# Performance work log

Measured on AMD Instinct MI355X. Metric: run time of the kernel, lower is better.

The kernel has to match this reference:

```python
import jax, jax.numpy as jnp
import numpy as np
from jax import lax

IMG = 224.0
IOU_THRESH = 0.5

def box_cxcywh_to_xyxy(b):
    cx, cy, w, h = b[..., 0], b[..., 1], b[..., 2], b[..., 3]
    return jnp.stack([cx - 0.5 * w, cy - 0.5 * h, cx + 0.5 * w, cy + 0.5 * h], axis=-1)

def box_iou(a, b):
    area_a = (a[:, 2] - a[:, 0]) * (a[:, 3] - a[:, 1])
    area_b = (b[:, 2] - b[:, 0]) * (b[:, 3] - b[:, 1])
    lt = jnp.maximum(a[:, None, :2], b[None, :, :2])
    rb = jnp.minimum(a[:, None, 2:], b[None, :, 2:])
    wh = jnp.clip(rb - lt, 0.0)
    inter = wh[..., 0] * wh[..., 1]
    return inter / (area_a[:, None] + area_b[None, :] - inter)

def gumbel_softmax(key, logits, axis, tau=1.0):
    # straight-through hard gumbel-softmax (matches torch hard=True)
    g = jax.random.gumbel(key, logits.shape, logits.dtype)
    y = jax.nn.softmax((logits + g) / tau, axis=axis)
    y_hard = jax.nn.one_hot(jnp.argmax(y, axis=axis), y.shape[axis], axis=axis, dtype=y.dtype)
    return y + lax.stop_gradient(y_hard - y)

def nms_indices(boxes, scores, thresh):
    # iterative greedy NMS, returns kept indices in descending-score order (as torchvision)
    n = boxes.shape[0]
    order = jnp.argsort(-scores)
    b = boxes[order]
    areas = (b[:, 2] - b[:, 0]) * (b[:, 3] - b[:, 1])
    pos = jnp.arange(n)
    def body(i, suppressed):
        bi = b[i]
        lt = jnp.maximum(bi[:2], b[:, :2])
        rb = jnp.minimum(bi[2:], b[:, 2:])
        wh = jnp.clip(rb - lt, 0.0)
        inter = wh[:, 0] * wh[:, 1]
        iou = inter / (areas[i] + areas - inter)
        sup = (iou > thresh) & (pos > i) & jnp.logical_not(suppressed[i])
        return suppressed | sup
    suppressed = lax.fori_loop(0, n, body, jnp.zeros((n,), bool))
    keep = np.asarray(jnp.logical_not(suppressed))
    return jnp.asarray(np.asarray(order)[keep])

def _keys():
    return jax.random.split(jax.random.key(42), 3)

def _boxes_and_scores(classencodings, pred_logits, pred_boxes, tgt_ids, batch_idx, tgt_bbox, k0):
    C = classencodings.shape[0]
    B, Q, D = pred_logits.shape
    similarity = jnp.einsum('bqd,cd->bqc', pred_logits, classencodings)
    out_scores = jnp.max(similarity, axis=-1)
    clt = gumbel_softmax(k0, similarity, axis=-1)                      # [B,Q,C] hard
    offx = jnp.arange(C, dtype=pred_logits.dtype) * IMG
    offy = jnp.arange(B, dtype=pred_logits.dtype) * IMG
    ox = jnp.sum(clt * offx, axis=-1)                                  # [B,Q]
    oy = jnp.broadcast_to(offy[:, None], (B, Q))
    out_off = jnp.tile(jnp.stack([ox, oy], axis=-1), (1, 1, 2))        # [B,Q,4]
    out_bbox = (box_cxcywh_to_xyxy(pred_boxes) + out_off).reshape(-1, 4)
    f = pred_logits.dtype
    gt_off = jnp.tile(jnp.stack([IMG * tgt_ids.astype(f), IMG * batch_idx.astype(f)], axis=-1), (1, 2))
    tb = box_cxcywh_to_xyxy(tgt_bbox) + gt_off                         # [N,4]
    return similarity, out_scores.reshape(-1), out_bbox, tb

def ce_diag(logits):
    # CrossEntropyLoss(mean) with targets arange(n)
    return -jnp.mean(jnp.diagonal(jax.nn.log_softmax(logits, axis=1)))

def _forward(classencodings, pred_logits, pred_boxes, pred_masks, tgt_masks, tgt_embs, tgt_bbox, tgt_ids, batch_idx, nms_idx):
    k0, k1, k2 = _keys()
    B, Q, D = pred_logits.shape
    N = tgt_embs.shape[0]
    W, H = tgt_masks.shape[-2:]
    similarity, out_scores, out_bbox, tb = _boxes_and_scores(classencodings, pred_logits, pred_boxes, tgt_ids, batch_idx, tgt_bbox, k0)
    kept = out_bbox[nms_idx]                                           # [K,4]
    K = kept.shape[0]
    iou = box_iou(kept, tb)
    iou = jnp.where(jnp.isnan(iou), 0.0, iou)
    gt_log = jax.nn.softmax(iou, axis=1)
    gt_one_hot = gumbel_softmax(k1, gt_log, axis=1)                    # [K,N]
    gt_sel = gt_one_hot.T @ kept                                       # [N,4]
    gt_ious = jnp.diagonal(box_iou(gt_sel, tb))
    out_embs = gt_one_hot.T @ pred_logits.reshape(-1, D)[nms_idx]      # [N,D]
    class_loss = ce_diag(tgt_embs @ out_embs.T) + ce_diag(out_embs @ tgt_embs.T)
    scores = jnp.einsum('bqd,nd->bqn', pred_logits, tgt_embs).reshape(B * Q, N)
    ind = gumbel_softmax(k2, scores, axis=0).T                         # [N,B*Q]
    om = (ind @ pred_masks.reshape(B * Q, -1)).reshape(N, W, H)
    overall_mask_loss = jnp.mean((om - tgt_masks) ** 2)
    ocm = jnp.einsum('qwh,bcq->bcwh', om, similarity) / om.shape[1]    # [B,Q,W,H] (N==C==Q)
    ocm = jax.nn.softmax(ocm, axis=1)
    batch_lookup = jax.nn.one_hot(batch_idx, B, dtype=pred_logits.dtype).T  # [B,N]
    gt_sim = tgt_embs @ classencodings.T                               # [N,C]
    tsim = batch_lookup[:, :, None] * gt_sim[None, :, :]               # [B,N,C]
    gt_cm = jnp.einsum('bnc,nwh->bcwh', tsim, tgt_masks)               # [B,C,W,H]
    inp = ocm.reshape(B, -1)
    tgt = gt_cm.reshape(B, -1)
    dice = jnp.mean(jnp.sum(inp * tgt) / (jnp.sum(inp, -1) + jnp.sum(tgt, -1) + 1e-6))
    l1 = jnp.abs(gt_sel - tb).sum()
    return jnp.stack([class_loss, dice, overall_mask_loss / K, (1.0 - gt_ious).sum() / K, l1 / K])

def setup_inputs():
    key = jax.random.key(0)
    ks = jax.random.split(key, 10)
    B, Q, C, N, D, W, H = 8, 300, 300, 300, 256, 96, 96
    return {
        'classencodings': jax.random.normal(ks[0], (C, D), jnp.float32),
        'pred_logits': jax.random.normal(ks[1], (B, Q, D), jnp.float32),
        'pred_boxes': jax.random.uniform(ks[2], (B, Q, 4), jnp.float32),
        'pred_masks': jax.random.normal(ks[3], (B * Q, W, H), jnp.float32),
        'tgt_masks': jax.random.uniform(ks[4], (N, W, H), jnp.float32),
        'tgt_embs': jax.random.normal(ks[5], (N, D), jnp.float32),
        'tgt_bbox': jax.random.uniform(ks[6], (N, 4), jnp.float32),
        'im_masks': jnp.ones((B, 224, 224), jnp.float32),
        'tgt_ids': jax.random.randint(ks[7], (N,), 0, C, jnp.int32),
        'batch_idx': jnp.sort(jax.random.randint(ks[8], (N,), 0, B, jnp.int32)),
    }

def reference(classencodings, pred_logits, pred_boxes, pred_masks, tgt_masks, tgt_embs, tgt_bbox, im_masks, tgt_ids, batch_idx):
    k0, _, _ = _keys()
    _, scores, out_bbox, _ = _boxes_and_scores(classencodings, pred_logits, pred_boxes, tgt_ids, batch_idx, tgt_bbox, k0)
    nms_idx = nms_indices(out_bbox, scores, IOU_THRESH)
    return _forward(classencodings, pred_logits, pred_boxes, pred_masks, tgt_masks, tgt_embs, tgt_bbox, tgt_ids, batch_idx, nms_idx)
```

## Files before the change

kernel.cpp:

```cpp
#include <hip/hip_runtime.h>
#include <stdint.h>

#define DEVFN __device__ __forceinline__

typedef unsigned short u16;
typedef short bf16x8 __attribute__((ext_vector_type(8)));
typedef float f32x4 __attribute__((ext_vector_type(4)));

constexpr int BB = 8, QQ = 300, CC = 300, NN = 300, DD = 256;
constexpr int WHX = 9216, BQ = 2400, SIMW = 600;
constexpr int QP = 320;
constexpr int CP = 304;
constexpr int KP = 96;
constexpr int NP = 416;
constexpr int CELLCAP = 300;

constexpr size_t F_SIMS   = 0;
constexpr size_t F_GTSIM  = F_SIMS   + (size_t)BQ*SIMW;
constexpr size_t F_MM     = F_GTSIM  + (size_t)NN*CC;
constexpr size_t F_SCORE  = F_MM     + (size_t)NN*NN;
constexpr size_t F_BBOX   = F_SCORE  + BQ;
constexpr size_t F_TB     = F_BBOX   + (size_t)BQ*4;
constexpr size_t F_SB     = F_TB     + (size_t)NN*4;
constexpr size_t F_SAREA  = F_SB     + (size_t)BQ*4;
constexpr size_t F_KB     = F_SAREA  + BQ;
constexpr size_t F_ROWSUM = F_KB     + (size_t)BQ*4;
constexpr size_t F_OE     = F_ROWSUM + NN;
constexpr size_t F_GSEL   = F_OE     + (size_t)NN*DD;
constexpr size_t F_MSUM   = F_GSEL   + (size_t)NN*4;
constexpr size_t F_STGT   = F_MSUM   + NN;
constexpr size_t F_SC     = F_STGT   + 8;
constexpr size_t F_CNT    = F_SC     + 16;
constexpr size_t F_ACCEND = F_CNT    + BQ;
constexpr size_t F_ORDER  = F_ACCEND;
constexpr size_t F_NMSIDX = F_ORDER  + BQ;
constexpr size_t F_SEL2   = F_NMSIDX + BQ;
constexpr size_t F_BSTART = F_SEL2   + NN;
constexpr size_t F_KINT   = F_BSTART + 16;
constexpr size_t F_CLS    = F_KINT   + 4;
constexpr size_t F_KEEPF  = F_CLS    + BQ;
constexpr size_t F_LIST   = F_KEEPF  + BQ;
constexpr size_t F_S2T    = F_LIST   + (size_t)BQ*CELLCAP;
constexpr size_t F_SIMTB  = ((F_S2T + (size_t)NN*BQ + 7) & ~(size_t)7);
constexpr size_t F_OMT    = F_SIMTB + (size_t)BB*CP*QP/2;
constexpr size_t F_TMT    = F_OMT   + (size_t)WHX*QP/2;
constexpr size_t F_GTP    = F_TMT   + (size_t)WHX*NP/2;
constexpr size_t F_TOTAL  = F_GTP   + (size_t)BB*CP*KP/2;

DEVFN uint32_t rotl32(uint32_t v, int r){ return (v << r) | (v >> (32 - r)); }

DEVFN void tf2x32(uint32_t k0, uint32_t k1, uint32_t x0, uint32_t x1,
                  uint32_t& o0, uint32_t& o1){
  uint32_t ks2 = k0 ^ k1 ^ 0x1BD11BDAu;
  x0 += k0; x1 += k1;
#define TFR(r) x0 += x1; x1 = rotl32(x1, r); x1 ^= x0;
  TFR(13) TFR(15) TFR(26) TFR(6)   x0 += k1;  x1 += ks2 + 1u;
  TFR(17) TFR(29) TFR(16) TFR(24)  x0 += ks2; x1 += k0  + 2u;
  TFR(13) TFR(15) TFR(26) TFR(6)   x0 += k0;  x1 += k1  + 3u;
  TFR(17) TFR(29) TFR(16) TFR(24)  x0 += k1;  x1 += ks2 + 4u;
  TFR(13) TFR(15) TFR(26) TFR(6)   x0 += ks2; x1 += k0  + 5u;
#undef TFR
  o0 = x0; o1 = x1;
}

DEVFN void subkey(int i, uint32_t& k0, uint32_t& k1){
  tf2x32(0u, 42u, 0u, (uint32_t)i, k0, k1);
}

DEVFN float gumbel32(uint32_t k0, uint32_t k1, uint32_t idx){
  uint32_t h, l; tf2x32(k0, k1, 0u, idx, h, l);
  uint32_t bits = h ^ l;
  float f = __uint_as_float((bits >> 9) | 0x3F800000u) - 1.0f;
  const float tiny = 1.17549435e-38f;
  float u = fmaxf(tiny, f + tiny);
  return -logf(-logf(u));
}

DEVFN float iou_xyxy(float ax1,float ay1,float ax2,float ay2,
                     float bx1,float by1,float bx2,float by2){
  float aa = (ax2-ax1)*(ay2-ay1);
  float ab = (bx2-bx1)*(by2-by1);
  float lx = fmaxf(ax1,bx1), ly = fmaxf(ay1,by1);
  float rx = fminf(ax2,bx2), ry = fminf(ay2,by2);
  float iw = fmaxf(rx-lx,0.f), ih = fmaxf(ry-ly,0.f);
  float in_ = iw*ih;
  return in_/(aa+ab-in_);
}

DEVFN u16 f2bf(float x){
  uint32_t u = __float_as_uint(x);
  uint32_t r = u + 0x7FFFu + ((u >> 16) & 1u);
  return (u16)(r >> 16);
}

DEVFN void gload_lds16(const u16* g, u16* l){
  __builtin_amdgcn_global_load_lds(
      (const __attribute__((address_space(1))) unsigned int*)g,
      (__attribute__((address_space(3))) unsigned int*)l,
      16, 0, 0);
}

__global__ __launch_bounds__(256) void k_gemm_t(
    const float* __restrict__ pl, const float* __restrict__ ce,
    const float* __restrict__ te, float* __restrict__ sims,
    float* __restrict__ gtsim, float* __restrict__ s2t){
  __shared__ float As[16][64];
  __shared__ float Bs[16][64];
  const int row0 = blockIdx.x * 64, col0 = blockIdx.y * 64;
  const int tid = threadIdx.x;
  const int lrow = tid >> 2, lk0 = (tid & 3) * 4;
  const int tr = tid >> 4, tc = tid & 15;

  float acc[4][4];
  #pragma unroll
  for (int i = 0; i < 4; i++)
    #pragma unroll
    for (int j = 0; j < 4; j++) acc[i][j] = 0.f;

  const float4 z4 = {0.f,0.f,0.f,0.f};
  const int grow = row0 + lrow;
  const int gcol = col0 + lrow;
  const float* arow = nullptr;
  if (grow < 2400) arow = pl + (size_t)grow * DD;
  else if (grow < 2700) arow = te + (size_t)(grow - 2400) * DD;
  const float* brow = nullptr;
  if (gcol < 300) brow = ce + (size_t)gcol * DD;
  else if (gcol < 600) brow = te + (size_t)(gcol - 300) * DD;

  float4 av = arow ? *(const float4*)(arow + lk0) : z4;
  float4 bv = brow ? *(const float4*)(brow + lk0) : z4;

  for (int step = 0; step < 16; step++){
    __syncthreads();
    #pragma unroll
    for (int j = 0; j < 4; j++){
      As[lk0 + j][lrow] = ((const float*)&av)[j];
      Bs[lk0 + j][lrow] = ((const float*)&bv)[j];
    }
    __syncthreads();
    if (step + 1 < 16){
      const int k0 = (step + 1) * 16;
      av = arow ? *(const float4*)(arow + k0 + lk0) : z4;
      bv = brow ? *(const float4*)(brow + k0 + lk0) : z4;
    }
    #pragma unroll
    for (int kk = 0; kk < 16; kk++){
      float4 a4 = *(const float4*)&As[kk][tr*4];
      float4 b4 = *(const float4*)&Bs[kk][tc*4];
      float a[4] = {a4.x,a4.y,a4.z,a4.w};
      float b[4] = {b4.x,b4.y,b4.z,b4.w};
      #pragma unroll
      for (int i = 0; i < 4; i++)
        #pragma unroll
        for (int j = 0; j < 4; j++)
          acc[i][j] = fmaf(a[i], b[j], acc[i][j]);
    }
  }

  #pragma unroll
  for (int i = 0; i < 4; i++){
    const int r = row0 + tr*4 + i;
    const int c0 = col0 + tc*4;
    if (r < 2400){
      if (c0 < 600){
        float4 o0 = {acc[i][0],acc[i][1],acc[i][2],acc[i][3]};
        *(float4*)(sims + (size_t)r*SIMW + c0) = o0;
        if (c0 >= 300){
          #pragma unroll
          for (int j = 0; j < 4; j++)
            s2t[(size_t)(c0 + j - 300)*BQ + r] = acc[i][j];
        }
      }
    } else if (r < 2700){
      const int n = r - 2400;
      #pragma unroll
      for (int j = 0; j < 4; j++){
        int c = c0 + j;
        if (c < 300) gtsim[(size_t)n*CC + c] = acc[i][j];
      }
    }
  }
}

__global__ __launch_bounds__(256) void k_post(
    const float* __restrict__ sims, const float* __restrict__ pb,
    const float* __restrict__ tbb, const int* __restrict__ tids,
    const int* __restrict__ bidx, const float* __restrict__ gtsim,
    float* __restrict__ score, float* __restrict__ bbox,
    float* __restrict__ tb, float* __restrict__ rowsum,
    int* __restrict__ clsout){
  int bq = blockIdx.x, tid = threadIdx.x;
  __shared__ float sv[256];
  __shared__ int   si[256];
  const int i2 = tid + 256;
  float v1 = (tid < CC) ? sims[(size_t)bq*SIMW + tid] : -INFINITY;
  float v2 = (i2  < CC) ? sims[(size_t)bq*SIMW + i2]  : -INFINITY;
  sv[tid] = fmaxf(v1, v2); __syncthreads();
  for (int s = 128; s > 0; s >>= 1){ if (tid < s) sv[tid] = fmaxf(sv[tid], sv[tid+s]); __syncthreads(); }
  if (tid == 0) score[bq] = sv[0];
  __syncthreads();
  uint32_t gk0, gk1; subkey(0, gk0, gk1);
  float y1 = (tid < CC) ? v1 + gumbel32(gk0, gk1, (uint32_t)(bq*CC + tid)) : -INFINITY;
  float y2 = (i2  < CC) ? v2 + gumbel32(gk0, gk1, (uint32_t)(bq*CC + i2))  : -INFINITY;
  float ym; int yi;
  if (y2 > y1){ ym = y2; yi = i2; } else { ym = y1; yi = tid; }
  sv[tid] = ym; si[tid] = yi; __syncthreads();
  for (int s = 128; s > 0; s >>= 1){
    if (tid < s){
      float ov = sv[tid+s]; int oi = si[tid+s];
      if (ov > sv[tid] || (ov == sv[tid] && oi < si[tid])){ sv[tid] = ov; si[tid] = oi; }
    }
    __syncthreads();
  }
  if (tid == 0){
    int cls = si[0];
    clsout[bq] = cls;
    float ox = 224.0f * (float)cls;
    float oy = 224.0f * (float)(bq / QQ);
    float cx = pb[bq*4+0], cy = pb[bq*4+1], ww = pb[bq*4+2], hh = pb[bq*4+3];
    bbox[bq*4+0] = cx - 0.5f*ww + ox;
    bbox[bq*4+1] = cy - 0.5f*hh + oy;
    bbox[bq*4+2] = cx + 0.5f*ww + ox;
    bbox[bq*4+3] = cy + 0.5f*hh + oy;
  }
  if (bq < NN){
    __syncthreads();
    float r1 = (tid < CC) ? gtsim[(size_t)bq*CC + tid] : 0.f;
    float r2 = (i2  < CC) ? gtsim[(size_t)bq*CC + i2]  : 0.f;
    sv[tid] = r1 + r2; __syncthreads();
    for (int s = 128; s > 0; s >>= 1){ if (tid < s) sv[tid] += sv[tid+s]; __syncthreads(); }
    if (tid == 0) rowsum[bq] = sv[0];
    if (tid == 1){
      float gx = 224.0f * (float)tids[bq], gy = 224.0f * (float)bidx[bq];
      float cx = tbb[bq*4+0], cy = tbb[bq*4+1], ww = tbb[bq*4+2], hh = tbb[bq*4+3];
      tb[bq*4+0] = cx - 0.5f*ww + gx;
      tb[bq*4+1] = cy - 0.5f*hh + gy;
      tb[bq*4+2] = cx + 0.5f*ww + gx;
      tb[bq*4+3] = cy + 0.5f*hh + gy;
    }
  }
}

__global__ __launch_bounds__(256) void k_rankgather(
    const float* __restrict__ score, const float* __restrict__ bbox,
    const int* __restrict__ cls, const int* __restrict__ bidx,
    int* __restrict__ order, float* __restrict__ sb,
    int* __restrict__ bstart, int* __restrict__ cnt,
    int* __restrict__ list){
  const int t = blockIdx.x;
  const int tid = threadIdx.x;
  const float st = score[t];
  int c = 0;
  for (int j = tid; j < BQ; j += 256){
    float sj = score[j];
    c += (sj > st) || (sj == st && j < t);
  }
  __shared__ int red[256];
  red[tid] = c; __syncthreads();
  for (int s = 128; s > 0; s >>= 1){
    if (tid < s) red[tid] += red[tid+s];
    __syncthreads();
  }
  if (tid == 0){
    int r = red[0];
    order[r] = t;
    float x1 = bbox[t*4+0], y1 = bbox[t*4+1], x2 = bbox[t*4+2], y2 = bbox[t*4+3];
    sb[r*4+0] = x1; sb[r*4+1] = y1; sb[r*4+2] = x2; sb[r*4+3] = y2;
    int key = (t / QQ) * CC + cls[t];
    int slot = atomicAdd(&cnt[key], 1);
    list[(size_t)key*CELLCAP + slot] = r;
  }
  if (t == 0 && tid >= 32 && tid < 41){
    int b = tid - 32, cb = 0;
    for (int n = 0; n < NN; n++) cb += (bidx[n] < b);
    bstart[b] = cb;
  }
}

__global__ __launch_bounds__(256) void k_cellnms(
    const float* __restrict__ sb, const int* __restrict__ cnt,
    const int* __restrict__ list, int* __restrict__ keepf){
  int key = blockIdx.x*256 + threadIdx.x;
  if (key >= BB*CC) return;
  int m = cnt[key];
  if (m <= 0) return;
  const int* lst = list + (size_t)key*CELLCAP;
  unsigned long long keptmask = 0ull;
  int prevp = -1;
  for (int a = 0; a < m; a++){
    int pa = 0x7fffffff;
    for (int j = 0; j < m; j++){
      int pj = lst[j];
      if (pj > prevp && pj < pa) pa = pj;
    }
    prevp = pa;
    float4 A = ((const float4*)sb)[pa];
    float areaA = (A.z-A.x)*(A.w-A.y);
    bool kept = true;
    int pbprev = -1;
    for (int b2 = 0; b2 < a; b2++){
      int pb = 0x7fffffff;
      for (int j = 0; j < m; j++){
        int pj = lst[j];
        if (pj > pbprev && pj < pb) pb = pj;
      }
      pbprev = pb;
      bool keptb = (m <= 64) ? (((keptmask >> b2) & 1ull) != 0ull) : (keepf[pb] != 0);
      if (!keptb) continue;
      float4 B = ((const float4*)sb)[pb];
      float areaB = (B.z-B.x)*(B.w-B.y);
      float lx = fmaxf(A.x,B.x), ly = fmaxf(A.y,B.y);
      float rx = fminf(A.z,B.z), ry = fminf(A.w,B.w);
      float iw = fmaxf(rx-lx,0.f), ih = fmaxf(ry-ly,0.f);
      float inter = iw*ih;
      if (inter/(areaA + areaB - inter) > 0.5f){ kept = false; break; }
    }
    if (m <= 64 && kept) keptmask |= (1ull << a);
    keepf[pa] = kept ? 1 : 0;
  }
}

__global__ __launch_bounds__(256) void k_compact(
    const int* __restrict__ keepflag, const int* __restrict__ order,
    const float* __restrict__ sb, int* __restrict__ nmsidx,
    float* __restrict__ kb, int* __restrict__ kint){
  __shared__ int csum[256];
  int tid = threadIdx.x;
  int p0 = tid*10;
  int keepf[10];
  int cnt = 0;
  #pragma unroll
  for (int d = 0; d < 10; d++){
    int p = p0 + d;
    int k = 0;
    if (p < BQ) k = keepflag[p];
    keepf[d] = k; cnt += k;
  }
  csum[tid] = cnt; __syncthreads();
  for (int s = 1; s < 256; s <<= 1){
    int add = (tid >= s) ? csum[tid - s] : 0;
    __syncthreads();
    csum[tid] += add;
    __syncthreads();
  }
  int pos = csum[tid] - cnt;
  #pragma unroll
  for (int d = 0; d < 10; d++){
    if (keepf[d]){
      int p = p0 + d;
      nmsidx[pos] = order[p];
      ((float4*)kb)[pos] = ((const float4*)sb)[p];
      pos++;
    }
  }
  if (tid == 255) kint[0] = csum[255];
}

__global__ __launch_bounds__(512) void k_gtsel(
    const float* __restrict__ kb, const float* __restrict__ tb,
    const int* __restrict__ nmsidx, const float* __restrict__ pl,
    const int* __restrict__ kint, float* __restrict__ gsel,
    float* __restrict__ oe){
  int k = blockIdx.x;
  if (k >= kint[0]) return;
  int tid = threadIdx.x;
  __shared__ float sv[512];
  __shared__ int   si[512];
  float4 a = ((const float4*)kb)[k];
  float iou = -INFINITY;
  if (tid < NN){
    float4 t = ((const float4*)tb)[tid];
    iou = iou_xyxy(a.x,a.y,a.z,a.w, t.x,t.y,t.z,t.w);
    if (iou != iou) iou = 0.f;
  }
  sv[tid] = iou; __syncthreads();
  for (int s = 256; s > 0; s >>= 1){ if (tid < s) sv[tid] = fmaxf(sv[tid], sv[tid+s]); __syncthreads(); }
  float m = sv[0]; __syncthreads();
  float e = (tid < NN) ? expf(iou - m) : 0.f;
  sv[tid] = e; __syncthreads();
  for (int s = 256; s > 0; s >>= 1){ if (tid < s) sv[tid] += sv[tid+s]; __syncthreads(); }
  float S = sv[0]; __syncthreads();
  uint32_t gk0, gk1; subkey(1, gk0, gk1);
  float y = (tid < NN) ? (e / S + gumbel32(gk0, gk1, (uint32_t)(k*NN + tid))) : -INFINITY;
  sv[tid] = y; si[tid] = tid; __syncthreads();
  for (int s = 256; s > 0; s >>= 1){
    if (tid < s){
      float ov = sv[tid+s]; int oi = si[tid+s];
      if (ov > sv[tid] || (ov == sv[tid] && oi < si[tid])){ sv[tid] = ov; si[tid] = oi; }
    }
    __syncthreads();
  }
  int sel = si[0];
  if (tid < 4) atomicAdd(&gsel[sel*4 + tid], ((const float*)&a)[tid]);
  if (tid < DD) atomicAdd(&oe[(size_t)sel*DD + tid], pl[(size_t)nmsidx[k]*DD + tid]);
}

__global__ __launch_bounds__(256) void k_m_t(
    const float* __restrict__ te, const float* __restrict__ oe,
    float* __restrict__ M){
  __shared__ float As[16][32];
  __shared__ float Bs[16][32];
  const int row0 = blockIdx.x * 32, col0 = blockIdx.y * 32;
  const int tid = threadIdx.x;
  const int lr = tid >> 3, lk0 = (tid & 7) * 2;
  const int tr = tid >> 4, tc = tid & 15;
  float acc[2][2] = {{0.f,0.f},{0.f,0.f}};
  const float* arow = (row0 + lr < NN) ? te + (size_t)(row0 + lr)*DD : nullptr;
  const float* brow = (col0 + lr < NN) ? oe + (size_t)(col0 + lr)*DD : nullptr;
  for (int step = 0; step < 16; step++){
    const int k0 = step*16;
    float2 a2 = arow ? *(const float2*)(arow + k0 + lk0) : float2{0.f,0.f};
    float2 b2 = brow ? *(const float2*)(brow + k0 + lk0) : float2{0.f,0.f};
    __syncthreads();
    As[lk0][lr] = a2.x; As[lk0+1][lr] = a2.y;
    Bs[lk0][lr] = b2.x; Bs[lk0+1][lr] = b2.y;
    __syncthreads();
    #pragma unroll
    for (int kk = 0; kk < 16; kk++){
      float a0 = As[kk][tr*2], a1 = As[kk][tr*2+1];
      float b0 = Bs[kk][tc*2], b1 = Bs[kk][tc*2+1];
      acc[0][0] = fmaf(a0,b0,acc[0][0]);
      acc[0][1] = fmaf(a0,b1,acc[0][1]);
      acc[1][0] = fmaf(a1,b0,acc[1][0]);
      acc[1][1] = fmaf(a1,b1,acc[1][1]);
    }
  }
  #pragma unroll
  for (int i = 0; i < 2; i++){
    int r = row0 + tr*2 + i;
    if (r >= NN) continue;
    #pragma unroll
    for (int j = 0; j < 2; j++){
      int c = col0 + tc*2 + j;
      if (c < NN) M[(size_t)r*NN + c] = acc[i][j];
    }
  }
}

__global__ __launch_bounds__(64) void k_ce(
    const float* __restrict__ M, float* __restrict__ sc){
  int i = blockIdx.x, lane = threadIdx.x;
  float m = -INFINITY;
  for (int j = lane; j < NN; j += 64) m = fmaxf(m, M[(size_t)i*NN + j]);
  for (int o = 32; o > 0; o >>= 1) m = fmaxf(m, __shfl_xor(m, o));
  float s = 0.f;
  for (int j = lane; j < NN; j += 64) s += expf(M[(size_t)i*NN + j] - m);
  for (int o = 32; o > 0; o >>= 1) s += __shfl_xor(s, o);
  float lr = m + logf(s);
  float m2 = -INFINITY;
  for (int j = lane; j < NN; j += 64) m2 = fmaxf(m2, M[(size_t)j*NN + i]);
  for (int o = 32; o > 0; o >>= 1) m2 = fmaxf(m2, __shfl_xor(m2, o));
  float s2 = 0.f;
  for (int j = lane; j < NN; j += 64) s2 += expf(M[(size_t)j*NN + i] - m2);
  for (int o = 32; o > 0; o >>= 1) s2 += __shfl_xor(s2, o);
  float lc = m2 + logf(s2);
  if (lane == 0){
    float d = M[(size_t)i*NN + i];
    atomicAdd(&sc[0], lr - d);
    atomicAdd(&sc[1], lc - d);
  }
}

__global__ __launch_bounds__(256) void k_sel2(
    const float* __restrict__ s2t, int* __restrict__ sel2){
  int n = blockIdx.x, tid = threadIdx.x;
  uint32_t gk0, gk1; subkey(2, gk0, gk1);
  float best = -INFINITY; int bi = 0x7fffffff;
  for (int r = tid; r < BQ; r += 256){
    float v = s2t[(size_t)n*BQ + r] + gumbel32(gk0, gk1, (uint32_t)(r*NN + n));
    if (v > best){ best = v; bi = r; }
  }
  __shared__ float sv[256];
  __shared__ int   si[256];
  sv[tid] = best; si[tid] = bi; __syncthreads();
  for (int s = 128; s > 0; s >>= 1){
    if (tid < s){
      float ov = sv[tid+s]; int oi = si[tid+s];
      if (ov > sv[tid] || (ov == sv[tid] && oi < si[tid])){ sv[tid] = ov; si[tid] = oi; }
    }
    __syncthreads();
  }
  if (tid == 0) sel2[n] = si[0];
}

constexpr int PB_SIMT = 400;
constexpr int PB_OMT  = 1440;
constexpr int PB_TMT  = 1872;
constexpr int PB_GTP  = 114;
constexpr int PB_OM   = 2700;
__global__ __launch_bounds__(256) void k_pack(
    const float* __restrict__ sims, const float* __restrict__ pm,
    const float* __restrict__ tm, const float* __restrict__ gtsim,
    const int* __restrict__ sel2, const int* __restrict__ bstart,
    u16* __restrict__ simTb, u16* __restrict__ omT,
    u16* __restrict__ tmT, u16* __restrict__ gtp,
    float* __restrict__ msum, float* __restrict__ sc){
  __shared__ float ld[32][65];
  const int blk = blockIdx.x;
  const int tid = threadIdx.x;

  if (blk < PB_SIMT){
    int bx = blk % 10, by = (blk / 10) % 5, b = blk / 50;
    int q0 = bx*32, c0 = by*64;
    for (int i = tid; i < 32*64; i += 256){
      int qi = i >> 6, ci = i & 63;
      int q = q0 + qi, c = c0 + ci;
      ld[qi][ci] = (q < QQ && c < CC) ? sims[((size_t)b*QQ + q)*SIMW + c] : 0.f;
    }
    __syncthreads();
    int cloc = tid >> 2, j0 = (tid & 3)*8;
    int c = c0 + cloc;
    if (c < CP){
      u16 tmp[8];
      #pragma unroll
      for (int j = 0; j < 8; j++) tmp[j] = f2bf(ld[j0+j][cloc]);
      *(uint4*)(simTb + ((size_t)b*CP + c)*QP + q0 + j0) = *(const uint4*)tmp;
    }
  } else if (blk < PB_SIMT + PB_OMT){
    int r = blk - PB_SIMT;
    int q0 = (r % 10)*32, wh0 = (r / 10)*64;
    for (int i = tid; i < 32*64; i += 256){
      int qi = i >> 6, wi = i & 63;
      int q = q0 + qi;
      ld[qi][wi] = (q < QQ) ? pm[(size_t)sel2[q]*WHX + wh0 + wi] * (1.0f/96.0f) : 0.f;
    }
    __syncthreads();
    int wloc = tid >> 2, j0 = (tid & 3)*8;
    u16 tmp[8];
    #pragma unroll
    for (int j = 0; j < 8; j++) tmp[j] = f2bf(ld[j0+j][wloc]);
    *(uint4*)(omT + (size_t)(wh0+wloc)*QP + q0 + j0) = *(const uint4*)tmp;
  } else if (blk < PB_SIMT + PB_OMT + PB_TMT){
    int r = blk - PB_SIMT - PB_OMT;
    int n0 = (r % 13)*32, wh0 = (r / 13)*64;
    for (int i = tid; i < 32*64; i += 256){
      int ni = i >> 6, wi = i & 63;
      int n = n0 + ni;
      ld[ni][wi] = (n < NN) ? tm[(size_t)n*WHX + wh0 + wi] : 0.f;
    }
    __syncthreads();
    int wloc = tid >> 2, j0 = (tid & 3)*8;
    u16 tmp[8];
    #pragma unroll
    for (int j = 0; j < 8; j++) tmp[j] = f2bf(ld[j0+j][wloc]);
    *(uint4*)(tmT + (size_t)(wh0+wloc)*NP + n0 + j0) = *(const uint4*)tmp;
  } else if (blk < PB_SIMT + PB_OMT + PB_TMT + PB_GTP){
    int g = (blk - PB_SIMT - PB_OMT - PB_TMT)*256 + tid;
    int b = g / (CP*(KP/8));
    int rem = g - b*(CP*(KP/8));
    int c = rem / (KP/8);
    int kg = rem % (KP/8);
    int n0 = bstart[b], n1 = bstart[b+1];
    int kst = n0 & ~7;
    u16 tmp[8];
    #pragma unroll
    for (int j = 0; j < 8; j++){
      int n = kst + kg*8 + j;
      float v = (n >= n0 && n < n1 && c < CC) ? gtsim[(size_t)n*CC + c] : 0.f;
      tmp[j] = f2bf(v);
    }
    *(uint4*)(gtp + ((size_t)b*CP + c)*KP + kg*8) = *(const uint4*)tmp;
  } else {
    int nb = blk - (PB_SIMT + PB_OMT + PB_TMT + PB_GTP);
    int n = nb / 9, ch = nb % 9;
    int c0 = ch*1024 + tid*4;
    const float4 o4 = *(const float4*)(pm + (size_t)sel2[n]*WHX + c0);
    const float4 t4 = *(const float4*)(tm + (size_t)n*WHX + c0);
    float dx = o4.x-t4.x, dy = o4.y-t4.y, dz = o4.z-t4.z, dw = o4.w-t4.w;
    float d2 = dx*dx + dy*dy + dz*dz + dw*dw;
    float ts = t4.x + t4.y + t4.z + t4.w;
    float* r1 = &ld[0][0];
    float* r2 = r1 + 256;
    r1[tid] = d2; r2[tid] = ts; __syncthreads();
    for (int s = 128; s > 0; s >>= 1){
      if (tid < s){ r1[tid] += r1[tid+s]; r2[tid] += r2[tid+s]; }
      __syncthreads();
    }
    if (tid == 0){ atomicAdd(&sc[2], r1[0]); atomicAdd(&msum[n], r2[0]); }
  }
}

constexpr int ALDS = 32;
__global__ __launch_bounds__(256) void k_zsoft(
    const u16* __restrict__ simTb, const u16* __restrict__ omT,
    const u16* __restrict__ gtp, const u16* __restrict__ tmT,
    const int* __restrict__ bstart, float* __restrict__ sc){
  const int bid = blockIdx.x;
  const int xcd = bid & 7;
  const int r9  = bid >> 3;
  const int tile = xcd * 18 + (r9 % 18);
  const int b    = r9 / 18;
  const int tid = threadIdx.x;
  const int w = tid >> 6, l = tid & 63;
  const int lrow = l & 15, lgrp = l >> 4;
  const int col = tile*64 + w*16 + lrow;

  __shared__ u16 As[2][CP*ALDS];
  __shared__ float red[256];

  const u16* Ab = simTb + (size_t)b*CP*QP;
  int srcoff[5];
  #pragma unroll
  for (int i = 0; i < 5; i++){
    int p = (w*5 + i)*64 + l;
    int row = p >> 2, cs = p & 3;
    int g = cs ^ ((row >> 1) & 3);
    srcoff[i] = row*QP + g*8;
  }
  const int nIss = (w == 3) ? 4 : 5;
  const int roff = (lgrp ^ ((lrow >> 1) & 3)) << 3;
  const u16* pB = omT + (size_t)col*QP + lgrp*8;

  #pragma unroll
  for (int i = 0; i < 5; i++){
    if (i < nIss) gload_lds16(Ab + srcoff[i], &As[0][(w*5+i)*512]);
  }
  bf16x8 bcur = *(const bf16x8*)(pB);

  f32x4 acc[19];
  #pragma unroll
  for (int t = 0; t < 19; t++) acc[t] = (f32x4){0.f,0.f,0.f,0.f};
  __syncthreads();

  for (int ks = 0; ks < 10; ks++){
    const int cur = ks & 1;
    bf16x8 bnext;
    if (ks + 1 < 10){
      const int ko = (ks + 1) * 32;
      #pragma unroll
      for (int i = 0; i < 5; i++){
        if (i < nIss) gload_lds16(Ab + srcoff[i] + ko, &As[cur ^ 1][(w*5+i)*512]);
      }
      bnext = *(const bf16x8*)(pB + ko);
    }
    __builtin_amdgcn_s_setprio(1);
    #pragma unroll
    for (int t = 0; t < 19; t++){
      bf16x8 af = *(const bf16x8*)&As[cur][t*16*ALDS + lrow*ALDS + roff];
      acc[t] = __builtin_amdgcn_mfma_f32_16x16x32_bf16(af, bcur, acc[t], 0, 0, 0);
    }
    __builtin_amdgcn_s_setprio(0);
    bcur = bnext;
    __syncthreads();
  }

  float lmax = -INFINITY;
  #pragma unroll
  for (int t = 0; t < 19; t++){
    if (t == 18 && lgrp == 3) continue;
    lmax = fmaxf(lmax, fmaxf(fmaxf(acc[t][0], acc[t][1]), fmaxf(acc[t][2], acc[t][3])));
  }
  lmax = fmaxf(lmax, __shfl_xor(lmax, 16));
  lmax = fmaxf(lmax, __shfl_xor(lmax, 32));
  float ls = 0.f;
  #pragma unroll
  for (int t = 0; t < 19; t++){
    if (t == 18 && lgrp == 3){
      acc[t] = (f32x4){0.f,0.f,0.f,0.f};
      continue;
    }
    float p0 = __expf(acc[t][0] - lmax);
    float p1 = __expf(acc[t][1] - lmax);
    float p2 = __expf(acc[t][2] - lmax);
    float p3 = __expf(acc[t][3] - lmax);
    acc[t][0] = p0; acc[t][1] = p1; acc[t][2] = p2; acc[t][3] = p3;
    ls += p0 + p1 + p2 + p3;
  }
  float S = ls;
  S += __shfl_xor(S, 16);
  S += __shfl_xor(S, 32);
  float inv = 1.f / S;

  const int n0 = bstart[b];
  const int kst = n0 & ~7;
  const u16* tB = tmT + (size_t)col*NP + kst + lgrp*8;
  bf16x8 b2a = *(const bf16x8*)(tB);
  bf16x8 b2b = *(const bf16x8*)(tB + 32);
  bf16x8 b2c = *(const bf16x8*)(tB + 64);
  const u16* A2 = gtp + (size_t)b*CP*KP + (size_t)lrow*KP + lgrp*8;
  float dl = 0.f;
  #pragma unroll
  for (int t = 0; t < 19; t++){
    const u16* ar = A2 + (size_t)t*16*KP;
    f32x4 rr = (f32x4){0.f,0.f,0.f,0.f};
    rr = __builtin_amdgcn_mfma_f32_16x16x32_bf16(*(const bf16x8*)(ar),      b2a, rr, 0, 0, 0);
    rr = __builtin_amdgcn_mfma_f32_16x16x32_bf16(*(const bf16x8*)(ar + 32), b2b, rr, 0, 0, 0);
    rr = __builtin_amdgcn_mfma_f32_16x16x32_bf16(*(const bf16x8*)(ar + 64), b2c, rr, 0, 0, 0);
    dl += acc[t][0]*rr[0] + acc[t][1]*rr[1] + acc[t][2]*rr[2] + acc[t][3]*rr[3];
  }
  dl *= inv;

  red[tid] = dl; __syncthreads();
  for (int s = 128; s > 0; s >>= 1){
    if (tid < s) red[tid] += red[tid+s];
    __syncthreads();
  }
  if (tid == 0) atomicAdd(&sc[5], red[0]);
}

__global__ __launch_bounds__(512) void k_final3(
    const float* __restrict__ gsel, const float* __restrict__ tb,
    const int* __restrict__ bidx, const float* __restrict__ rowsum,
    const float* __restrict__ msum, const float* __restrict__ sc,
    const int* __restrict__ kint, float* __restrict__ out){
  int tid = threadIdx.x;
  __shared__ float s1[512], s2[512];
  __shared__ float stgt[8];
  if (tid < 8) stgt[tid] = 0.f;
  __syncthreads();
  float a1 = 0.f, a2 = 0.f;
  if (tid < NN){
    float4 g = ((const float4*)gsel)[tid];
    float4 t = ((const float4*)tb)[tid];
    float iou = iou_xyxy(g.x,g.y,g.z,g.w, t.x,t.y,t.z,t.w);
    a1 = 1.f - iou;
    a2 = fabsf(g.x-t.x) + fabsf(g.y-t.y) + fabsf(g.z-t.z) + fabsf(g.w-t.w);
    atomicAdd(&stgt[bidx[tid]], rowsum[tid] * msum[tid]);
  }
  s1[tid] = a1; s2[tid] = a2; __syncthreads();
  for (int s = 256; s > 0; s >>= 1){
    if (tid < s){ s1[tid] += s1[tid+s]; s2[tid] += s2[tid+s]; }
    __syncthreads();
  }
  if (tid == 0){
    float K = (float)kint[0];
    float cls = sc[0]/300.f + sc[1]/300.f;
    float stot = sc[5];
    float dice = 0.f;
    for (int b = 0; b < 8; b++) dice += stot / (9216.0f + stgt[b] + 1e-6f);
    dice *= (1.0f/8.0f);
    out[0] = cls;
    out[1] = dice;
    out[2] = (sc[2] / 2764800.0f) / K;
    out[3] = s1[0] / K;
    out[4] = s2[0] / K;
  }
}

extern "C" void kernel_launch(void* const* d_in, const int* in_sizes, int n_in,
                              void* d_out, int out_size, void* d_ws, size_t ws_size,
                              hipStream_t stream) {
  const float* ce  = (const float*)d_in[0];
  const float* pl  = (const float*)d_in[1];
  const float* pb  = (const float*)d_in[2];
  const float* pm  = (const float*)d_in[3];
  const float* tm  = (const float*)d_in[4];
  const float* te  = (const float*)d_in[5];
  const float* tbb = (const float*)d_in[6];
  const int*  tids = (const int*)d_in[8];
  const int*  bidx = (const int*)d_in[9];
  float* out = (float*)d_out;
  float* w = (float*)d_ws;

  if (ws_size < F_TOTAL * sizeof(float)) return;

  float* SIMS   = w + F_SIMS;
  float* GTSIM  = w + F_GTSIM;
  float* MM     = w + F_MM;
  float* SCORE  = w + F_SCORE;
  float* BBOX   = w + F_BBOX;
  float* TBOX   = w + F_TB;
  float* SB     = w + F_SB;
  float* KB     = w + F_KB;
  float* ROWSUM = w + F_ROWSUM;
  float* OE     = w + F_OE;
  float* GSEL   = w + F_GSEL;
  float* MSUM   = w + F_MSUM;
  float* SC     = w + F_SC;
  float* S2T    = w + F_S2T;
  int*   CNT    = (int*)(w + F_CNT);
  int*   ORDER  = (int*)(w + F_ORDER);
  int*   NMSIDX = (int*)(w + F_NMSIDX);
  int*   SEL2   = (int*)(w + F_SEL2);
  int*   BSTART = (int*)(w + F_BSTART);
  int*   KINT   = (int*)(w + F_KINT);
  int*   CLS    = (int*)(w + F_CLS);
  int*   KEEPF  = (int*)(w + F_KEEPF);
  int*   LIST   = (int*)(w + F_LIST);
  u16* SIMTB = (u16*)(w + F_SIMTB);
  u16* OMT   = (u16*)(w + F_OMT);
  u16* TMT   = (u16*)(w + F_TMT);
  u16* GTP   = (u16*)(w + F_GTP);

  hipMemsetAsync(w + F_OE, 0, (F_ACCEND - F_OE) * sizeof(float), stream);

  k_gemm_t<<<dim3(43, 10), 256, 0, stream>>>(pl, ce, te, SIMS, GTSIM, S2T);
  k_post<<<BQ, 256, 0, stream>>>(SIMS, pb, tbb, tids, bidx, GTSIM, SCORE, BBOX, TBOX, ROWSUM, CLS);
  k_rankgather<<<BQ, 256, 0, stream>>>(SCORE, BBOX, CLS, bidx, ORDER, SB, BSTART, CNT, LIST);
  k_sel2<<<NN, 256, 0, stream>>>(S2T, SEL2);
  k_pack<<<PB_SIMT + PB_OMT + PB_TMT + PB_GTP + PB_OM, 256, 0, stream>>>(
      SIMS, pm, tm, GTSIM, SEL2, BSTART, SIMTB, OMT, TMT, GTP, MSUM, SC);
  k_cellnms<<<(BB*CC + 255)/256, 256, 0, stream>>>(SB, CNT, LIST, KEEPF);
  k_compact<<<1, 256, 0, stream>>>(KEEPF, ORDER, SB, NMSIDX, KB, KINT);
  k_gtsel<<<BQ, 512, 0, stream>>>(KB, TBOX, NMSIDX, pl, KINT, GSEL, OE);
  k_m_t<<<dim3(10, 10), 256, 0, stream>>>(te, OE, MM);
  k_ce<<<NN, 64, 0, stream>>>(MM, SC);
  k_zsoft<<<dim3((WHX/64) * BB), 256, 0, stream>>>(SIMTB, OMT, GTP, TMT, BSTART, SC);
  k_final3<<<1, 512, 0, stream>>>(GSEL, TBOX, bidx, ROWSUM, MSUM, SC, KINT, out);
}
```

Measured before the change: 248.5 us.

## Load zsoft GEMM A-operand directly from global instead of LDS double buffer

Removes the LDS double-buffered staging of the A operand (with its XOR swizzle, async global-to-LDS copies, barriers and priority hints) in the zsoft kernel. Each wave now reads its A fragments straight from global memory per k-step. This cuts LDS traffic, barriers and LDS occupancy pressure. The cost is redundant global/L2 reads across the four waves, which previously shared the tile, and no prefetch overlap.

```diff
diff --git a/kernel.cpp b/kernel.cpp
--- a/kernel.cpp
+++ b/kernel.cpp
@@ -93,13 +93,6 @@
   return (u16)(r >> 16);
 }
 
-DEVFN void gload_lds16(const u16* g, u16* l){
-  __builtin_amdgcn_global_load_lds(
-      (const __attribute__((address_space(1))) unsigned int*)g,
-      (__attribute__((address_space(3))) unsigned int*)l,
-      16, 0, 0);
-}
-
 __global__ __launch_bounds__(256) void k_gemm_t(
     const float* __restrict__ pl, const float* __restrict__ ce,
     const float* __restrict__ te, float* __restrict__ sims,
@@ -580,7 +573,6 @@
   }
 }
 
-constexpr int ALDS = 32;
 __global__ __launch_bounds__(256) void k_zsoft(
     const u16* __restrict__ simTb, const u16* __restrict__ omT,
     const u16* __restrict__ gtp, const u16* __restrict__ tmT,
@@ -595,53 +587,23 @@
   const int lrow = l & 15, lgrp = l >> 4;
   const int col = tile*64 + w*16 + lrow;
 
-  __shared__ u16 As[2][CP*ALDS];
   __shared__ float red[256];
 
-  const u16* Ab = simTb + (size_t)b*CP*QP;
-  int srcoff[5];
-  #pragma unroll
-  for (int i = 0; i < 5; i++){
-    int p = (w*5 + i)*64 + l;
-    int row = p >> 2, cs = p & 3;
-    int g = cs ^ ((row >> 1) & 3);
-    srcoff[i] = row*QP + g*8;
-  }
-  const int nIss = (w == 3) ? 4 : 5;
-  const int roff = (lgrp ^ ((lrow >> 1) & 3)) << 3;
+  const u16* Ab = simTb + (size_t)b*CP*QP + (size_t)lrow*QP + lgrp*8;
   const u16* pB = omT + (size_t)col*QP + lgrp*8;
 
-  #pragma unroll
-  for (int i = 0; i < 5; i++){
-    if (i < nIss) gload_lds16(Ab + srcoff[i], &As[0][(w*5+i)*512]);
-  }
-  bf16x8 bcur = *(const bf16x8*)(pB);
-
   f32x4 acc[19];
   #pragma unroll
   for (int t = 0; t < 19; t++) acc[t] = (f32x4){0.f,0.f,0.f,0.f};
-  __syncthreads();
 
   for (int ks = 0; ks < 10; ks++){
-    const int cur = ks & 1;
-    bf16x8 bnext;
-    if (ks + 1 < 10){
-      const int ko = (ks + 1) * 32;
-      #pragma unroll
-      for (int i = 0; i < 5; i++){
-        if (i < nIss) gload_lds16(Ab + srcoff[i] + ko, &As[cur ^ 1][(w*5+i)*512]);
-      }
-      bnext = *(const bf16x8*)(pB + ko);
-    }
-    __builtin_amdgcn_s_setprio(1);
+    const int ko = ks * 32;
+    bf16x8 bcur = *(const bf16x8*)(pB + ko);
     #pragma unroll
     for (int t = 0; t < 19; t++){
-      bf16x8 af = *(const bf16x8*)&As[cur][t*16*ALDS + lrow*ALDS + roff];
+      bf16x8 af = *(const bf16x8*)(Ab + (size_t)t*16*QP + ko);
       acc[t] = __builtin_amdgcn_mfma_f32_16x16x32_bf16(af, bcur, acc[t], 0, 0, 0);
     }
-    __builtin_amdgcn_s_setprio(0);
-    bcur = bnext;
-    __syncthreads();
   }
 
   float lmax = -INFINITY;
```

Result: slower. 335.4 us (+35.0%).
